# Kernel optimization log

Measured on AMD Instinct MI355X. Metric: run time of the kernel, lower is better.

The kernel has to match this reference:

```python
import jax, jax.numpy as jnp
import numpy as np

N = 100_000        # PPI nodes
F_IN = 512         # num_features
H1, H2 = 16, 32    # GCN hidden / out channels
E = 3_200_000      # edges
NUM_DRUGS = 1024
B = 4096           # DDI batch rows


def setup_inputs() -> dict:
    key = jax.random.key(0)
    ks = jax.random.split(key, 16)
    s = 0.05
    return {
        "x": jax.random.normal(ks[0], (N, F_IN), jnp.float32),
        "edge_index": jax.random.randint(ks[1], (2, E), 0, N, dtype=jnp.int64),
        "DDI_feature": jax.random.normal(ks[2], (B, NUM_DRUGS + H2), jnp.float32),
        "W1": jax.random.normal(ks[3], (F_IN, H1), jnp.float32) * s,
        "b1": jax.random.normal(ks[4], (H1,), jnp.float32) * s,
        "W2": jax.random.normal(ks[5], (H1, H2), jnp.float32) * s,
        "b2": jax.random.normal(ks[6], (H2,), jnp.float32) * s,
        "fW1": jax.random.normal(ks[7], (NUM_DRUGS + H2, 64), jnp.float32) * s,
        "fb1": jax.random.normal(ks[8], (64,), jnp.float32) * s,
        "fW2": jax.random.normal(ks[9], (64, 16), jnp.float32) * s,
        "fb2": jax.random.normal(ks[10], (16,), jnp.float32) * s,
        "fW3": jax.random.normal(ks[11], (16, 1), jnp.float32) * s,
        "fb3": jax.random.normal(ks[12], (1,), jnp.float32) * s,
    }


def _gcn_conv(x, src, dst, W, b):
    """torch_geometric GCNConv with add_self_loops=True, symmetric norm.
    lin -> D^{-1/2} (A + I) D^{-1/2} -> + bias."""
    h = x @ W                                   # [N, out] linear first (faithful to GCNConv)
    ones = jnp.ones(src.shape[0], h.dtype)
    deg = jax.ops.segment_sum(ones, dst, num_segments=N) + 1.0  # +1 self-loop
    dinv = jax.lax.rsqrt(deg)                   # deg > 0 guaranteed by self-loop
    norm = dinv[src] * dinv[dst]                # [E]
    agg = jax.ops.segment_sum(h[src] * norm[:, None], dst, num_segments=N)
    agg = agg + h * (dinv * dinv)[:, None]      # self-loop message, norm = 1/deg
    return agg + b


def reference(x, edge_index, DDI_feature, W1, b1, W2, b2, fW1, fb1, fW2, fb2, fW3, fb3):
    src, dst = edge_index[0], edge_index[1]
    # PPI branch: conv1 -> relu -> (dropout: eval mode = identity) -> conv2 -> relu
    ppi = jax.nn.relu(_gcn_conv(x, src, dst, W1, b1))
    ppi = jax.nn.relu(_gcn_conv(ppi, src, dst, W2, b2))          # [N, 32]
    # DDI branch: fc1 -> relu -> fc2 -> relu -> fc3 -> relu
    ddi = jax.nn.relu(DDI_feature @ fW1 + fb1)
    ddi = jax.nn.relu(ddi @ fW2 + fb2)
    ddi = jax.nn.relu(ddi @ fW3 + fb3)                           # [B, 1]
    return ppi, ddi
```

## Files before the change

### kernel.cpp

```cpp
#include <hip/hip_runtime.h>

#define N_NODES 100000
#define HALF_N  50000
#define FEAT_IN 512
#define C1 16
#define C2 32
#define NEDGE 3200000
#define B_DDI 4096
#define F_DDI 1056

#define NBUCK 196
#define CAP_BUCK 32768
#define BIN_C 6144
#define NB_BIN ((NEDGE + BIN_C - 1) / BIN_C)
#define PB_CAP 12288

typedef float f4v __attribute__((ext_vector_type(4)));

#define O_DINV   0u
#define O_RP2    524288u
#define O_COL    1572864u
#define O_GBUF   16777216u
#define O_H1     46137344u
#define O_OUT1   54525952u
#define O_GCUR   71303168u


__global__ __launch_bounds__(256) void k_bin(const int* __restrict__ ei,
                                             int* __restrict__ gcur,
                                             unsigned int* __restrict__ gbuf) {
    __shared__ int lcnt[256];
    __shared__ int lscan[256];
    __shared__ int lbase[256];
    __shared__ unsigned int sdat[BIN_C];
    __shared__ unsigned char sb[BIN_C];
    int tid = threadIdx.x;
    int e0 = blockIdx.x * BIN_C;

    lcnt[tid] = 0;
    __syncthreads();
    #pragma unroll 4
    for (int j = 0; j < BIN_C / 256; ++j) {
        int e = e0 + j * 256 + tid;
        if (e < NEDGE) atomicAdd(&lcnt[ei[NEDGE + e] >> 9], 1);
    }
    __syncthreads();
    lscan[tid] = lcnt[tid];
    __syncthreads();
    for (int off = 1; off < 256; off <<= 1) {
        int t = (tid >= off) ? lscan[tid - off] : 0;
        __syncthreads();
        lscan[tid] += t;
        __syncthreads();
    }
    lscan[tid] -= lcnt[tid];
    if (tid < NBUCK) lbase[tid] = tid * CAP_BUCK + atomicAdd(&gcur[tid], lcnt[tid]);
    __syncthreads();
    lcnt[tid] = 0;
    __syncthreads();
    #pragma unroll 4
    for (int j = 0; j < BIN_C / 256; ++j) {
        int e = e0 + j * 256 + tid;
        if (e < NEDGE) {
            int s = ei[e];
            int d = ei[NEDGE + e];
            int b = d >> 9;
            int p = lscan[b] + atomicAdd(&lcnt[b], 1);
            sdat[p] = (unsigned int)s | ((unsigned int)(d & 511) << 17);
            sb[p] = (unsigned char)b;
        }
    }
    __syncthreads();
    int tot = (e0 + BIN_C <= NEDGE) ? BIN_C : (NEDGE - e0);
    for (int i = tid; i < tot; i += 256) {
        int b = sb[i];
        gbuf[lbase[b] + (i - lscan[b])] = sdat[i];
    }
}

__global__ __launch_bounds__(512) void k_place(const int* __restrict__ gcur,
                                               const unsigned int* __restrict__ gbuf,
                                               int* __restrict__ col,
                                               int* __restrict__ rp2,
                                               float* __restrict__ dinv) {
    __shared__ int scat[PB_CAP];
    __shared__ int pre[256];
    __shared__ int cnt2[1024];
    __shared__ int sc[512];
    __shared__ int lcur[1024];
    int b = blockIdx.x;
    int tid = threadIdx.x;

    if (tid < 256) pre[tid] = (tid < NBUCK) ? gcur[tid] : 0;
    __syncthreads();
    for (int off = 1; off < 256; off <<= 1) {
        int t = 0;
        if (tid < 256 && tid >= off) t = pre[tid - off];
        __syncthreads();
        if (tid < 256) pre[tid] += t;
        __syncthreads();
    }
    int Eb = gcur[b];
    int begc = pre[b] - Eb;
    if (b == NBUCK - 1 && tid == 0) rp2[2 * N_NODES] = NEDGE;
    const unsigned int* __restrict__ gb = gbuf + ((size_t)b << 15);
    int n0 = b * 512;

    cnt2[tid] = 0; cnt2[tid + 512] = 0;
    __syncthreads();
    for (int i = tid; i < Eb; i += 512) {
        unsigned int u = gb[i];
        int dl = (int)(u >> 17);
        int src = (int)(u & 0x1FFFFu);
        atomicAdd(&cnt2[dl * 2 + (src >= HALF_N)], 1);
    }
    __syncthreads();
    int a = cnt2[2 * tid], bb = cnt2[2 * tid + 1];
    sc[tid] = a + bb;
    __syncthreads();
    for (int off = 1; off < 512; off <<= 1) {
        int t = (tid >= off) ? sc[tid - off] : 0;
        __syncthreads();
        sc[tid] += t;
        __syncthreads();
    }
    int ex = sc[tid] - (a + bb);
    lcur[2 * tid] = ex;
    lcur[2 * tid + 1] = ex + a;
    int n = n0 + tid;
    if (n < N_NODES) {
        rp2[2 * n] = begc + ex;
        rp2[2 * n + 1] = begc + ex + a;
        dinv[n] = rsqrtf((float)(a + bb) + 1.0f);
    }
    __syncthreads();
    int h0 = sc[255];

    if (h0 <= PB_CAP && (Eb - h0) <= PB_CAP) {
        for (int i = tid; i < Eb; i += 512) {
            unsigned int u = gb[i];
            int dl = (int)(u >> 17);
            int src = (int)(u & 0x1FFFFu);
            if (dl < 256) {
                int p = atomicAdd(&lcur[dl * 2 + (src >= HALF_N)], 1);
                scat[p] = src;
            }
        }
        __syncthreads();
        for (int i = tid; i < h0; i += 512) col[begc + i] = scat[i];
        __syncthreads();
        for (int i = tid; i < Eb; i += 512) {
            unsigned int u = gb[i];
            int dl = (int)(u >> 17);
            int src = (int)(u & 0x1FFFFu);
            if (dl >= 256) {
                int p = atomicAdd(&lcur[dl * 2 + (src >= HALF_N)], 1);
                scat[p - h0] = src;
            }
        }
        __syncthreads();
        for (int i = tid; i < Eb - h0; i += 512) col[begc + h0 + i] = scat[i];
    } else {
        for (int i = tid; i < Eb; i += 512) {
            unsigned int u = gb[i];
            int dl = (int)(u >> 17);
            int src = (int)(u & 0x1FFFFu);
            int p = atomicAdd(&lcur[dl * 2 + (src >= HALF_N)], 1);
            col[begc + p] = src;
        }
    }
}


__global__ __launch_bounds__(256) void k_gemm1(const float* __restrict__ x,
                                               const float* __restrict__ W1,
                                               const float* __restrict__ dinv,
                                               float* __restrict__ h1s) {
    __shared__ float part[4][64][17];
    int tid = threadIdx.x;
    int wv = __builtin_amdgcn_readfirstlane(tid >> 6);
    int lane = tid & 63;
    int row = blockIdx.x * 64 + lane;
    int crow = row < N_NODES ? row : N_NODES - 1;
    const float* __restrict__ xr = x + (size_t)crow * FEAT_IN + wv * 128;

    float acc[16];
    #pragma unroll
    for (int c = 0; c < 16; ++c) acc[c] = 0.f;

    for (int it = 0; it < 8; ++it) {
        const float4* xp = reinterpret_cast<const float4*>(xr + it * 16);
        float4 xv0 = xp[0], xv1 = xp[1], xv2 = xp[2], xv3 = xp[3];
        float xs[16] = {xv0.x, xv0.y, xv0.z, xv0.w, xv1.x, xv1.y, xv1.z, xv1.w,
                        xv2.x, xv2.y, xv2.z, xv2.w, xv3.x, xv3.y, xv3.z, xv3.w};
        int kb = wv * 128 + it * 16;
        #pragma unroll
        for (int j = 0; j < 16; ++j) {
            const float* __restrict__ wr = W1 + (size_t)(kb + j) * 16;
            #pragma unroll
            for (int c = 0; c < 16; ++c) acc[c] = fmaf(xs[j], wr[c], acc[c]);
        }
    }
    #pragma unroll
    for (int c = 0; c < 16; ++c) part[wv][lane][c] = acc[c];
    __syncthreads();

    int r2 = tid >> 2, cq = tid & 3;
    int grow = blockIdx.x * 64 + r2;
    if (grow < N_NODES) {
        float dv = dinv[grow];
        float o[4];
        #pragma unroll
        for (int j = 0; j < 4; ++j) {
            int c = cq * 4 + j;
            o[j] = dv * (part[0][r2][c] + part[1][r2][c] + part[2][r2][c] + part[3][r2][c]);
        }
        *reinterpret_cast<float4*>(&h1s[(size_t)grow * C1 + cq * 4]) =
            make_float4(o[0], o[1], o[2], o[3]);
    }
}


__global__ __launch_bounds__(256) void k_gather1(const int* __restrict__ rp2, const int* __restrict__ col,
                                                 const float* __restrict__ dinv, const float* __restrict__ h1s,
                                                 const float* __restrict__ b1, float* __restrict__ out1s) {
    int t = blockIdx.x * 256 + threadIdx.x;
    int node = t >> 2;
    int q = t & 3;
    if (node >= N_NODES) return;
    int beg = rp2[2 * node], end = rp2[2 * node + 2];
    f4v acc = {0.f, 0.f, 0.f, 0.f};
    int p = beg;
    while (p < end && (p & 3)) {
        int s = col[p++];
        acc += *reinterpret_cast<const f4v*>(&h1s[s * C1 + q * 4]);
    }
    for (; p + 7 < end; p += 8) {
        int4 sa = *reinterpret_cast<const int4*>(&col[p]);
        int4 sb = *reinterpret_cast<const int4*>(&col[p + 4]);
        f4v v0 = *reinterpret_cast<const f4v*>(&h1s[sa.x * C1 + q * 4]);
        f4v v1 = *reinterpret_cast<const f4v*>(&h1s[sa.y * C1 + q * 4]);
        f4v v2 = *reinterpret_cast<const f4v*>(&h1s[sa.z * C1 + q * 4]);
        f4v v3 = *reinterpret_cast<const f4v*>(&h1s[sa.w * C1 + q * 4]);
        f4v v4 = *reinterpret_cast<const f4v*>(&h1s[sb.x * C1 + q * 4]);
        f4v v5 = *reinterpret_cast<const f4v*>(&h1s[sb.y * C1 + q * 4]);
        f4v v6 = *reinterpret_cast<const f4v*>(&h1s[sb.z * C1 + q * 4]);
        f4v v7 = *reinterpret_cast<const f4v*>(&h1s[sb.w * C1 + q * 4]);
        acc += ((v0 + v1) + (v2 + v3)) + ((v4 + v5) + (v6 + v7));
    }
    for (; p + 3 < end; p += 4) {
        int4 sa = *reinterpret_cast<const int4*>(&col[p]);
        f4v v0 = *reinterpret_cast<const f4v*>(&h1s[sa.x * C1 + q * 4]);
        f4v v1 = *reinterpret_cast<const f4v*>(&h1s[sa.y * C1 + q * 4]);
        f4v v2 = *reinterpret_cast<const f4v*>(&h1s[sa.z * C1 + q * 4]);
        f4v v3 = *reinterpret_cast<const f4v*>(&h1s[sa.w * C1 + q * 4]);
        acc += (v0 + v1) + (v2 + v3);
    }
    for (; p < end; ++p) {
        int s = col[p];
        acc += *reinterpret_cast<const f4v*>(&h1s[s * C1 + q * 4]);
    }
    float di = dinv[node];
    f4v hs = *reinterpret_cast<const f4v*>(&h1s[node * C1 + q * 4]);
    f4v bv = *reinterpret_cast<const f4v*>(&b1[q * 4]);
    f4v v = di * (acc + hs) + bv;
    f4v z = {0.f, 0.f, 0.f, 0.f};
    f4v r = v > z ? v : z;
    *reinterpret_cast<f4v*>(&out1s[node * C1 + q * 4]) = di * r;
}

__global__ __launch_bounds__(256) void k_gather2(const int* __restrict__ rp2, const int* __restrict__ col,
                                                 const float* __restrict__ dinv, const float* __restrict__ out1s,
                                                 const float* __restrict__ W2, const float* __restrict__ b2,
                                                 float* __restrict__ out) {
    __shared__ float sacc[64][17];
    __shared__ float sW[16 * 32];
    __shared__ float sb2[32];
    int tid = threadIdx.x;
    if (tid < 128)
        *reinterpret_cast<float4*>(&sW[tid * 4]) = *reinterpret_cast<const float4*>(&W2[tid * 4]);
    if (tid < 32) sb2[tid] = b2[tid];
    int g = tid >> 2;
    int q = tid & 3;
    int nodeRaw = blockIdx.x * 64 + g;
    int node = nodeRaw < N_NODES ? nodeRaw : N_NODES - 1;
    int beg = rp2[2 * node], end = rp2[2 * node + 2];
    f4v acc = {0.f, 0.f, 0.f, 0.f};
    int p = beg;
    while (p < end && (p & 3)) {
        int s = col[p++];
        acc += *reinterpret_cast<const f4v*>(&out1s[s * C1 + q * 4]);
    }
    for (; p + 7 < end; p += 8) {
        int4 sa = *reinterpret_cast<const int4*>(&col[p]);
        int4 sb = *reinterpret_cast<const int4*>(&col[p + 4]);
        f4v v0 = *reinterpret_cast<const f4v*>(&out1s[sa.x * C1 + q * 4]);
        f4v v1 = *reinterpret_cast<const f4v*>(&out1s[sa.y * C1 + q * 4]);
        f4v v2 = *reinterpret_cast<const f4v*>(&out1s[sa.z * C1 + q * 4]);
        f4v v3 = *reinterpret_cast<const f4v*>(&out1s[sa.w * C1 + q * 4]);
        f4v v4 = *reinterpret_cast<const f4v*>(&out1s[sb.x * C1 + q * 4]);
        f4v v5 = *reinterpret_cast<const f4v*>(&out1s[sb.y * C1 + q * 4]);
        f4v v6 = *reinterpret_cast<const f4v*>(&out1s[sb.z * C1 + q * 4]);
        f4v v7 = *reinterpret_cast<const f4v*>(&out1s[sb.w * C1 + q * 4]);
        acc += ((v0 + v1) + (v2 + v3)) + ((v4 + v5) + (v6 + v7));
    }
    for (; p + 3 < end; p += 4) {
        int4 sa = *reinterpret_cast<const int4*>(&col[p]);
        f4v v0 = *reinterpret_cast<const f4v*>(&out1s[sa.x * C1 + q * 4]);
        f4v v1 = *reinterpret_cast<const f4v*>(&out1s[sa.y * C1 + q * 4]);
        f4v v2 = *reinterpret_cast<const f4v*>(&out1s[sa.z * C1 + q * 4]);
        f4v v3 = *reinterpret_cast<const f4v*>(&out1s[sa.w * C1 + q * 4]);
        acc += (v0 + v1) + (v2 + v3);
    }
    for (; p < end; ++p) {
        int s = col[p];
        acc += *reinterpret_cast<const f4v*>(&out1s[s * C1 + q * 4]);
    }
    float di = dinv[node];
    f4v hs = *reinterpret_cast<const f4v*>(&out1s[node * C1 + q * 4]);
    f4v v = di * (acc + hs);
    sacc[g][q * 4 + 0] = v.x;
    sacc[g][q * 4 + 1] = v.y;
    sacc[g][q * 4 + 2] = v.z;
    sacc[g][q * 4 + 3] = v.w;
    __syncthreads();
    float r[8];
    #pragma unroll
    for (int j = 0; j < 8; ++j) r[j] = sb2[q * 8 + j];
    #pragma unroll
    for (int k = 0; k < 16; ++k) {
        float a = sacc[g][k];
        const float* wrow = &sW[k * 32 + q * 8];
        #pragma unroll
        for (int j = 0; j < 8; ++j) r[j] = fmaf(a, wrow[j], r[j]);
    }
    if (nodeRaw < N_NODES) {
        f4v z = {0.f, 0.f, 0.f, 0.f};
        f4v o0 = {r[0], r[1], r[2], r[3]};
        f4v o1 = {r[4], r[5], r[6], r[7]};
        o0 = o0 > z ? o0 : z;
        o1 = o1 > z ? o1 : z;
        *reinterpret_cast<f4v*>(&out[nodeRaw * C2 + q * 8]) = o0;
        *reinterpret_cast<f4v*>(&out[nodeRaw * C2 + q * 8 + 4]) = o1;
    }
}


#define DDI_CHUNK 132

__global__ __launch_bounds__(256) void k_ddi(const float* __restrict__ feat,
                                             const float* __restrict__ fW1, const float* __restrict__ fb1,
                                             const float* __restrict__ fW2, const float* __restrict__ fb2,
                                             const float* __restrict__ fW3, const float* __restrict__ fb3,
                                             float* __restrict__ out) {
    __shared__ float sW[DDI_CHUNK * 64];
    __shared__ float sH[4][64];
    int tid = threadIdx.x;
    int wave = tid >> 6;
    int lane = tid & 63;
    int row = blockIdx.x * 4 + wave;

    float acc = 0.f;
    for (int k0 = 0; k0 < F_DDI; k0 += DDI_CHUNK) {
        __syncthreads();
        for (int idx = tid; idx < DDI_CHUNK * 64; idx += 256)
            sW[idx] = fW1[k0 * 64 + idx];
        __syncthreads();
        const float* frow = &feat[(size_t)row * F_DDI + k0];
        #pragma unroll 4
        for (int kk = 0; kk < DDI_CHUNK; kk += 4) {
            float4 fv = *reinterpret_cast<const float4*>(&frow[kk]);
            acc += fv.x * sW[(kk + 0) * 64 + lane];
            acc += fv.y * sW[(kk + 1) * 64 + lane];
            acc += fv.z * sW[(kk + 2) * 64 + lane];
            acc += fv.w * sW[(kk + 3) * 64 + lane];
        }
    }
    float h = fmaxf(acc + fb1[lane], 0.f);
    __syncthreads();
    sH[wave][lane] = h;
    __syncthreads();

    int c16 = lane & 15;
    float acc2 = 0.f;
    #pragma unroll
    for (int kk = 0; kk < 64; ++kk)
        acc2 += sH[wave][kk] * fW2[kk * 16 + c16];
    float o2 = fmaxf(acc2 + fb2[c16], 0.f);
    float part = o2 * fW3[c16];
    #pragma unroll
    for (int off = 8; off >= 1; off >>= 1)
        part += __shfl_xor(part, off, 16);
    if (lane == 0)
        out[row] = fmaxf(part + fb3[0], 0.f);
}


extern "C" void kernel_launch(void* const* d_in, const int* in_sizes, int n_in,
                              void* d_out, int out_size, void* d_ws, size_t ws_size,
                              hipStream_t stream) {
    const float* x   = (const float*)d_in[0];
    const int*   ei  = (const int*)d_in[1];
    const float* ddi = (const float*)d_in[2];
    const float* W1  = (const float*)d_in[3];
    const float* b1  = (const float*)d_in[4];
    const float* W2  = (const float*)d_in[5];
    const float* b2  = (const float*)d_in[6];
    const float* fW1 = (const float*)d_in[7];
    const float* fb1 = (const float*)d_in[8];
    const float* fW2 = (const float*)d_in[9];
    const float* fb2 = (const float*)d_in[10];
    const float* fW3 = (const float*)d_in[11];
    const float* fb3 = (const float*)d_in[12];

    char* ws = (char*)d_ws;
    float* dinv  = (float*)(ws + O_DINV);
    int*   rp2   = (int*)(ws + O_RP2);
    int*   col   = (int*)(ws + O_COL);
    unsigned int* gbuf = (unsigned int*)(ws + O_GBUF);
    float* h1s   = (float*)(ws + O_H1);
    float* out1s = (float*)(ws + O_OUT1);
    int*   gcur  = (int*)(ws + O_GCUR);

    float* out_ppi = (float*)d_out;
    float* out_ddi = out_ppi + (size_t)N_NODES * C2;

    hipMemsetAsync(gcur, 0, NBUCK * sizeof(int), stream);
    k_bin<<<NB_BIN, 256, 0, stream>>>(ei, gcur, gbuf);
    k_place<<<NBUCK, 512, 0, stream>>>(gcur, gbuf, col, rp2, dinv);

    k_gemm1<<<(N_NODES + 63) / 64, 256, 0, stream>>>(x, W1, dinv, h1s);

    int gblk = (N_NODES * 4 + 255) / 256;
    k_gather1<<<gblk, 256, 0, stream>>>(rp2, col, dinv, h1s, b1, out1s);
    k_gather2<<<(N_NODES + 63) / 64, 256, 0, stream>>>(rp2, col, dinv, out1s, W2, b2, out_ppi);

    k_ddi<<<B_DDI / 4, 256, 0, stream>>>(ddi, fW1, fb1, fW2, fb2, fW3, fb3, out_ddi);
}
```

Baseline: 282.0 us.

## Sort nodes by degree within buckets to balance gather wavefront work

Replaces the CSR row-pointer array with a per-bucket permutation of nodes ordered by in-degree (counting sort on a 128-bin histogram), storing packed node id plus degree and a begin offset per slot. The gather kernels walk slots in this order, so lanes in a wavefront handle nodes with similar degree and diverge less. The old split of each node's edges by source half (src >= HALF_N) is dropped, which simplifies placement. In exchange, output writes become scattered by node id, k_place gains an extra histogram/scan, and more slots are launched, including padding slots.

```diff
diff --git a/kernel.cpp b/kernel.cpp
--- a/kernel.cpp
+++ b/kernel.cpp
@@ -1,7 +1,6 @@
 #include <hip/hip_runtime.h>
 
 #define N_NODES 100000
-#define HALF_N  50000
 #define FEAT_IN 512
 #define C1 16
 #define C2 32
@@ -10,15 +9,18 @@
 #define F_DDI 1056
 
 #define NBUCK 196
+#define NSLOT (NBUCK * 512)
 #define CAP_BUCK 32768
 #define BIN_C 6144
 #define NB_BIN ((NEDGE + BIN_C - 1) / BIN_C)
 #define PB_CAP 12288
+#define INVALID_N 0x1FFFFu
 
 typedef float f4v __attribute__((ext_vector_type(4)));
 
 #define O_DINV   0u
-#define O_RP2    524288u
+#define O_PND    524288u
+#define O_PBEG   925696u
 #define O_COL    1572864u
 #define O_GBUF   16777216u
 #define O_H1     46137344u
@@ -81,13 +83,17 @@
 __global__ __launch_bounds__(512) void k_place(const int* __restrict__ gcur,
                                                const unsigned int* __restrict__ gbuf,
                                                int* __restrict__ col,
-                                               int* __restrict__ rp2,
+                                               unsigned int* __restrict__ pnd,
+                                               int* __restrict__ pbeg,
                                                float* __restrict__ dinv) {
     __shared__ int scat[PB_CAP];
     __shared__ int pre[256];
-    __shared__ int cnt2[1024];
+    __shared__ int cnt[512];
     __shared__ int sc[512];
-    __shared__ int lcur[1024];
+    __shared__ int lcur[512];
+    __shared__ int hist[128];
+    __shared__ int hbase[128];
+    __shared__ int hcur[128];
     int b = blockIdx.x;
     int tid = threadIdx.x;
 
@@ -102,21 +108,17 @@
     }
     int Eb = gcur[b];
     int begc = pre[b] - Eb;
-    if (b == NBUCK - 1 && tid == 0) rp2[2 * N_NODES] = NEDGE;
     const unsigned int* __restrict__ gb = gbuf + ((size_t)b << 15);
     int n0 = b * 512;
 
-    cnt2[tid] = 0; cnt2[tid + 512] = 0;
-    __syncthreads();
-    for (int i = tid; i < Eb; i += 512) {
-        unsigned int u = gb[i];
-        int dl = (int)(u >> 17);
-        int src = (int)(u & 0x1FFFFu);
-        atomicAdd(&cnt2[dl * 2 + (src >= HALF_N)], 1);
-    }
-    __syncthreads();
-    int a = cnt2[2 * tid], bb = cnt2[2 * tid + 1];
-    sc[tid] = a + bb;
+    cnt[tid] = 0;
+    if (tid < 128) { hist[tid] = 0; hcur[tid] = 0; }
+    __syncthreads();
+    for (int i = tid; i < Eb; i += 512)
+        atomicAdd(&cnt[gb[i] >> 17], 1);
+    __syncthreads();
+    int deg = cnt[tid];
+    sc[tid] = deg;
     __syncthreads();
     for (int off = 1; off < 512; off <<= 1) {
         int t = (tid >= off) ? sc[tid - off] : 0;
@@ -124,26 +126,38 @@
         sc[tid] += t;
         __syncthreads();
     }
-    int ex = sc[tid] - (a + bb);
-    lcur[2 * tid] = ex;
-    lcur[2 * tid + 1] = ex + a;
+    int ex = sc[tid] - deg;
+    lcur[tid] = ex;
     int n = n0 + tid;
-    if (n < N_NODES) {
-        rp2[2 * n] = begc + ex;
-        rp2[2 * n + 1] = begc + ex + a;
-        dinv[n] = rsqrtf((float)(a + bb) + 1.0f);
-    }
-    __syncthreads();
+    bool valid = n < N_NODES;
+    if (valid) dinv[n] = rsqrtf((float)deg + 1.0f);
+
+    int dc = deg < 127 ? deg : 127;
+    atomicAdd(&hist[dc], 1);
+    __syncthreads();
+    if (tid < 128) hbase[tid] = hist[tid];
+    __syncthreads();
+    for (int off = 1; off < 128; off <<= 1) {
+        int t = 0;
+        if (tid < 128 && tid >= off) t = hbase[tid - off];
+        __syncthreads();
+        if (tid < 128) hbase[tid] += t;
+        __syncthreads();
+    }
+    int rank = (hbase[dc] - hist[dc]) + atomicAdd(&hcur[dc], 1);
+    int slot = n0 + rank;
+    pnd[slot] = valid ? ((unsigned int)n | ((unsigned int)deg << 17)) : INVALID_N;
+    pbeg[slot] = begc + ex;
+    __syncthreads();
+
     int h0 = sc[255];
-
     if (h0 <= PB_CAP && (Eb - h0) <= PB_CAP) {
         for (int i = tid; i < Eb; i += 512) {
             unsigned int u = gb[i];
             int dl = (int)(u >> 17);
-            int src = (int)(u & 0x1FFFFu);
             if (dl < 256) {
-                int p = atomicAdd(&lcur[dl * 2 + (src >= HALF_N)], 1);
-                scat[p] = src;
+                int p = atomicAdd(&lcur[dl], 1);
+                scat[p] = (int)(u & 0x1FFFFu);
             }
         }
         __syncthreads();
@@ -152,10 +166,9 @@
         for (int i = tid; i < Eb; i += 512) {
             unsigned int u = gb[i];
             int dl = (int)(u >> 17);
-            int src = (int)(u & 0x1FFFFu);
             if (dl >= 256) {
-                int p = atomicAdd(&lcur[dl * 2 + (src >= HALF_N)], 1);
-                scat[p - h0] = src;
+                int p = atomicAdd(&lcur[dl], 1);
+                scat[p - h0] = (int)(u & 0x1FFFFu);
             }
         }
         __syncthreads();
@@ -163,10 +176,8 @@
     } else {
         for (int i = tid; i < Eb; i += 512) {
             unsigned int u = gb[i];
-            int dl = (int)(u >> 17);
-            int src = (int)(u & 0x1FFFFu);
-            int p = atomicAdd(&lcur[dl * 2 + (src >= HALF_N)], 1);
-            col[begc + p] = src;
+            int p = atomicAdd(&lcur[u >> 17], 1);
+            col[begc + p] = (int)(u & 0x1FFFFu);
         }
     }
 }
@@ -221,14 +232,20 @@
 }
 
 
-__global__ __launch_bounds__(256) void k_gather1(const int* __restrict__ rp2, const int* __restrict__ col,
-                                                 const float* __restrict__ dinv, const float* __restrict__ h1s,
-                                                 const float* __restrict__ b1, float* __restrict__ out1s) {
+__global__ __launch_bounds__(256) void k_gather1(const unsigned int* __restrict__ pnd,
+                                                 const int* __restrict__ pbeg,
+                                                 const int* __restrict__ col,
+                                                 const float* __restrict__ dinv,
+                                                 const float* __restrict__ h1s,
+                                                 const float* __restrict__ b1,
+                                                 float* __restrict__ out1s) {
     int t = blockIdx.x * 256 + threadIdx.x;
-    int node = t >> 2;
+    int slot = t >> 2;
     int q = t & 3;
+    unsigned int pn = pnd[slot];
+    int node = (int)(pn & 0x1FFFFu);
     if (node >= N_NODES) return;
-    int beg = rp2[2 * node], end = rp2[2 * node + 2];
+    int beg = pbeg[slot], end = beg + (int)(pn >> 17);
     f4v acc = {0.f, 0.f, 0.f, 0.f};
     int p = beg;
     while (p < end && (p & 3)) {
@@ -269,9 +286,13 @@
     *reinterpret_cast<f4v*>(&out1s[node * C1 + q * 4]) = di * r;
 }
 
-__global__ __launch_bounds__(256) void k_gather2(const int* __restrict__ rp2, const int* __restrict__ col,
-                                                 const float* __restrict__ dinv, const float* __restrict__ out1s,
-                                                 const float* __restrict__ W2, const float* __restrict__ b2,
+__global__ __launch_bounds__(256) void k_gather2(const unsigned int* __restrict__ pnd,
+                                                 const int* __restrict__ pbeg,
+                                                 const int* __restrict__ col,
+                                                 const float* __restrict__ dinv,
+                                                 const float* __restrict__ out1s,
+                                                 const float* __restrict__ W2,
+                                                 const float* __restrict__ b2,
                                                  float* __restrict__ out) {
     __shared__ float sacc[64][17];
     __shared__ float sW[16 * 32];
@@ -282,9 +303,13 @@
     if (tid < 32) sb2[tid] = b2[tid];
     int g = tid >> 2;
     int q = tid & 3;
-    int nodeRaw = blockIdx.x * 64 + g;
-    int node = nodeRaw < N_NODES ? nodeRaw : N_NODES - 1;
-    int beg = rp2[2 * node], end = rp2[2 * node + 2];
+    int slot = blockIdx.x * 64 + g;
+    unsigned int pn = pnd[slot];
+    int node = (int)(pn & 0x1FFFFu);
+    bool valid = node < N_NODES;
+    int nodeC = valid ? node : 0;
+    int beg = pbeg[slot];
+    int end = valid ? beg + (int)(pn >> 17) : beg;
     f4v acc = {0.f, 0.f, 0.f, 0.f};
     int p = beg;
     while (p < end && (p & 3)) {
@@ -316,8 +341,8 @@
         int s = col[p];
         acc += *reinterpret_cast<const f4v*>(&out1s[s * C1 + q * 4]);
     }
-    float di = dinv[node];
-    f4v hs = *reinterpret_cast<const f4v*>(&out1s[node * C1 + q * 4]);
+    float di = dinv[nodeC];
+    f4v hs = *reinterpret_cast<const f4v*>(&out1s[nodeC * C1 + q * 4]);
     f4v v = di * (acc + hs);
     sacc[g][q * 4 + 0] = v.x;
     sacc[g][q * 4 + 1] = v.y;
@@ -334,14 +359,14 @@
         #pragma unroll
         for (int j = 0; j < 8; ++j) r[j] = fmaf(a, wrow[j], r[j]);
     }
-    if (nodeRaw < N_NODES) {
+    if (valid) {
         f4v z = {0.f, 0.f, 0.f, 0.f};
         f4v o0 = {r[0], r[1], r[2], r[3]};
         f4v o1 = {r[4], r[5], r[6], r[7]};
         o0 = o0 > z ? o0 : z;
         o1 = o1 > z ? o1 : z;
-        *reinterpret_cast<f4v*>(&out[nodeRaw * C2 + q * 8]) = o0;
-        *reinterpret_cast<f4v*>(&out[nodeRaw * C2 + q * 8 + 4]) = o1;
+        *reinterpret_cast<f4v*>(&out[node * C2 + q * 8]) = o0;
+        *reinterpret_cast<f4v*>(&out[node * C2 + q * 8 + 4]) = o1;
     }
 }
 
@@ -415,7 +440,8 @@
 
     char* ws = (char*)d_ws;
     float* dinv  = (float*)(ws + O_DINV);
-    int*   rp2   = (int*)(ws + O_RP2);
+    unsigned int* pnd = (unsigned int*)(ws + O_PND);
+    int*   pbeg  = (int*)(ws + O_PBEG);
     int*   col   = (int*)(ws + O_COL);
     unsigned int* gbuf = (unsigned int*)(ws + O_GBUF);
     float* h1s   = (float*)(ws + O_H1);
@@ -427,13 +453,12 @@
 
     hipMemsetAsync(gcur, 0, NBUCK * sizeof(int), stream);
     k_bin<<<NB_BIN, 256, 0, stream>>>(ei, gcur, gbuf);
-    k_place<<<NBUCK, 512, 0, stream>>>(gcur, gbuf, col, rp2, dinv);
+    k_place<<<NBUCK, 512, 0, stream>>>(gcur, gbuf, col, pnd, pbeg, dinv);
 
     k_gemm1<<<(N_NODES + 63) / 64, 256, 0, stream>>>(x, W1, dinv, h1s);
 
-    int gblk = (N_NODES * 4 + 255) / 256;
-    k_gather1<<<gblk, 256, 0, stream>>>(rp2, col, dinv, h1s, b1, out1s);
-    k_gather2<<<(N_NODES + 63) / 64, 256, 0, stream>>>(rp2, col, dinv, out1s, W2, b2, out_ppi);
+    k_gather1<<<NSLOT * 4 / 256, 256, 0, stream>>>(pnd, pbeg, col, dinv, h1s, b1, out1s);
+    k_gather2<<<NSLOT / 64, 256, 0, stream>>>(pnd, pbeg, col, dinv, out1s, W2, b2, out_ppi);
 
     k_ddi<<<B_DDI / 4, 256, 0, stream>>>(ddi, fW1, fb1, fW2, fb2, fW3, fb3, out_ddi);
 }
```

New measurement: 305.5 us. +8.3%, slower.

## Drop source-half edge split in CSR build and process four DDI rows per wave

Applied to the files above, without the earlier changes.

The CSR placement kernel no longer partitions each node's incoming edges by whether the source is in the lower or upper half of the node range. It uses a single counter per node, which cuts shared atomics and index math. The second row pointer is set equal to the first, so downstream gathers treat the first half as empty, which may lose the locality the split gave or change behaviour. The DDI MLP kernel now computes four rows per wave, so each loaded weight chunk is reused across 16 rows per block and quarter as many blocks re-stage fW1.

```diff
diff --git a/kernel.cpp b/kernel.cpp
--- a/kernel.cpp
+++ b/kernel.cpp
@@ -1,7 +1,6 @@
 #include <hip/hip_runtime.h>
 
 #define N_NODES 100000
-#define HALF_N  50000
 #define FEAT_IN 512
 #define C1 16
 #define C2 32
@@ -85,9 +84,9 @@
                                                float* __restrict__ dinv) {
     __shared__ int scat[PB_CAP];
     __shared__ int pre[256];
-    __shared__ int cnt2[1024];
+    __shared__ int cnt[512];
     __shared__ int sc[512];
-    __shared__ int lcur[1024];
+    __shared__ int lcur[512];
     int b = blockIdx.x;
     int tid = threadIdx.x;
 
@@ -106,17 +105,13 @@
     const unsigned int* __restrict__ gb = gbuf + ((size_t)b << 15);
     int n0 = b * 512;
 
-    cnt2[tid] = 0; cnt2[tid + 512] = 0;
-    __syncthreads();
-    for (int i = tid; i < Eb; i += 512) {
-        unsigned int u = gb[i];
-        int dl = (int)(u >> 17);
-        int src = (int)(u & 0x1FFFFu);
-        atomicAdd(&cnt2[dl * 2 + (src >= HALF_N)], 1);
-    }
-    __syncthreads();
-    int a = cnt2[2 * tid], bb = cnt2[2 * tid + 1];
-    sc[tid] = a + bb;
+    cnt[tid] = 0;
+    __syncthreads();
+    for (int i = tid; i < Eb; i += 512)
+        atomicAdd(&cnt[gb[i] >> 17], 1);
+    __syncthreads();
+    int deg = cnt[tid];
+    sc[tid] = deg;
     __syncthreads();
     for (int off = 1; off < 512; off <<= 1) {
         int t = (tid >= off) ? sc[tid - off] : 0;
@@ -124,14 +119,13 @@
         sc[tid] += t;
         __syncthreads();
     }
-    int ex = sc[tid] - (a + bb);
-    lcur[2 * tid] = ex;
-    lcur[2 * tid + 1] = ex + a;
+    int ex = sc[tid] - deg;
+    lcur[tid] = ex;
     int n = n0 + tid;
     if (n < N_NODES) {
         rp2[2 * n] = begc + ex;
-        rp2[2 * n + 1] = begc + ex + a;
-        dinv[n] = rsqrtf((float)(a + bb) + 1.0f);
+        rp2[2 * n + 1] = begc + ex;
+        dinv[n] = rsqrtf((float)deg + 1.0f);
     }
     __syncthreads();
     int h0 = sc[255];
@@ -140,10 +134,9 @@
         for (int i = tid; i < Eb; i += 512) {
             unsigned int u = gb[i];
             int dl = (int)(u >> 17);
-            int src = (int)(u & 0x1FFFFu);
             if (dl < 256) {
-                int p = atomicAdd(&lcur[dl * 2 + (src >= HALF_N)], 1);
-                scat[p] = src;
+                int p = atomicAdd(&lcur[dl], 1);
+                scat[p] = (int)(u & 0x1FFFFu);
             }
         }
         __syncthreads();
@@ -152,10 +145,9 @@
         for (int i = tid; i < Eb; i += 512) {
             unsigned int u = gb[i];
             int dl = (int)(u >> 17);
-            int src = (int)(u & 0x1FFFFu);
             if (dl >= 256) {
-                int p = atomicAdd(&lcur[dl * 2 + (src >= HALF_N)], 1);
-                scat[p - h0] = src;
+                int p = atomicAdd(&lcur[dl], 1);
+                scat[p - h0] = (int)(u & 0x1FFFFu);
             }
         }
         __syncthreads();
@@ -163,10 +155,8 @@
     } else {
         for (int i = tid; i < Eb; i += 512) {
             unsigned int u = gb[i];
-            int dl = (int)(u >> 17);
-            int src = (int)(u & 0x1FFFFu);
-            int p = atomicAdd(&lcur[dl * 2 + (src >= HALF_N)], 1);
-            col[begc + p] = src;
+            int p = atomicAdd(&lcur[u >> 17], 1);
+            col[begc + p] = (int)(u & 0x1FFFFu);
         }
     }
 }
@@ -354,45 +344,50 @@
                                              const float* __restrict__ fW3, const float* __restrict__ fb3,
                                              float* __restrict__ out) {
     __shared__ float sW[DDI_CHUNK * 64];
-    __shared__ float sH[4][64];
+    __shared__ float sH[4][4][64];
     int tid = threadIdx.x;
     int wave = tid >> 6;
     int lane = tid & 63;
-    int row = blockIdx.x * 4 + wave;
-
-    float acc = 0.f;
+    int row0 = blockIdx.x * 16 + wave * 4;
+
+    float acc[4] = {0.f, 0.f, 0.f, 0.f};
     for (int k0 = 0; k0 < F_DDI; k0 += DDI_CHUNK) {
         __syncthreads();
         for (int idx = tid; idx < DDI_CHUNK * 64; idx += 256)
             sW[idx] = fW1[k0 * 64 + idx];
         __syncthreads();
-        const float* frow = &feat[(size_t)row * F_DDI + k0];
-        #pragma unroll 4
-        for (int kk = 0; kk < DDI_CHUNK; kk += 4) {
-            float4 fv = *reinterpret_cast<const float4*>(&frow[kk]);
-            acc += fv.x * sW[(kk + 0) * 64 + lane];
-            acc += fv.y * sW[(kk + 1) * 64 + lane];
-            acc += fv.z * sW[(kk + 2) * 64 + lane];
-            acc += fv.w * sW[(kk + 3) * 64 + lane];
-        }
-    }
-    float h = fmaxf(acc + fb1[lane], 0.f);
-    __syncthreads();
-    sH[wave][lane] = h;
-    __syncthreads();
-
+        #pragma unroll
+        for (int r = 0; r < 4; ++r) {
+            const float* frow = &feat[(size_t)(row0 + r) * F_DDI + k0];
+            #pragma unroll 4
+            for (int kk = 0; kk < DDI_CHUNK; kk += 4) {
+                float4 fv = *reinterpret_cast<const float4*>(&frow[kk]);
+                acc[r] += fv.x * sW[(kk + 0) * 64 + lane];
+                acc[r] += fv.y * sW[(kk + 1) * 64 + lane];
+                acc[r] += fv.z * sW[(kk + 2) * 64 + lane];
+                acc[r] += fv.w * sW[(kk + 3) * 64 + lane];
+            }
+        }
+    }
+    float bl = fb1[lane];
+    #pragma unroll
+    for (int r = 0; r < 4; ++r)
+        sH[wave][r][lane] = fmaxf(acc[r] + bl, 0.f);
+    __syncthreads();
+
+    int rg = lane >> 4;
     int c16 = lane & 15;
     float acc2 = 0.f;
     #pragma unroll
     for (int kk = 0; kk < 64; ++kk)
-        acc2 += sH[wave][kk] * fW2[kk * 16 + c16];
+        acc2 += sH[wave][rg][kk] * fW2[kk * 16 + c16];
     float o2 = fmaxf(acc2 + fb2[c16], 0.f);
     float part = o2 * fW3[c16];
     #pragma unroll
     for (int off = 8; off >= 1; off >>= 1)
         part += __shfl_xor(part, off, 16);
-    if (lane == 0)
-        out[row] = fmaxf(part + fb3[0], 0.f);
+    if (c16 == 0)
+        out[row0 + rg] = fmaxf(part + fb3[0], 0.f);
 }
 
 
@@ -435,5 +430,5 @@
     k_gather1<<<gblk, 256, 0, stream>>>(rp2, col, dinv, h1s, b1, out1s);
     k_gather2<<<(N_NODES + 63) / 64, 256, 0, stream>>>(rp2, col, dinv, out1s, W2, b2, out_ppi);
 
-    k_ddi<<<B_DDI / 4, 256, 0, stream>>>(ddi, fW1, fb1, fW2, fb2, fW3, fb3, out_ddi);
-}
+    k_ddi<<<B_DDI / 16, 256, 0, stream>>>(ddi, fW1, fb1, fW2, fb2, fW3, fb3, out_ddi);
+}
```

Result: slower. 360.0 us (+27.7%).
